# Performance work log

Hardware: AMD Instinct MI355X
Metric: run time of the kernel (lower is better)

The kernel has to match this reference:

```python
import jax, jax.numpy as jnp
import numpy as np

C_Z = 128
C_H = 128
N = 512
B = 1

def _layer_norm(x, g, b, eps=1e-5):
    mu = jnp.mean(x, axis=-1, keepdims=True)
    var = jnp.var(x, axis=-1, keepdims=True)
    return (x - mu) * jax.lax.rsqrt(var + eps) * g + b

def _linear(x, w, b):
    # torch Linear: y = x @ w.T + b, w: [out, in]
    return jnp.einsum('...i,oi->...o', x, w) + b

def setup_inputs() -> dict:
    key = jax.random.key(0)
    ks = jax.random.split(key, 8)
    s = 1.0 / np.sqrt(C_Z)
    return {
        'z': jax.random.normal(ks[0], (B, N, N, C_Z), jnp.float32),
        'mask': jnp.ones((B, N, N), jnp.float32),
        'ln_in_g': jnp.ones((C_Z,), jnp.float32),
        'ln_in_b': jnp.zeros((C_Z,), jnp.float32),
        'w_ag': jax.random.normal(ks[1], (C_H, C_Z), jnp.float32) * s,
        'b_ag': jnp.ones((C_H,), jnp.float32),
        'w_ap': jax.random.normal(ks[2], (C_H, C_Z), jnp.float32) * s,
        'b_ap': jnp.zeros((C_H,), jnp.float32),
        'w_bg': jax.random.normal(ks[3], (C_H, C_Z), jnp.float32) * s,
        'b_bg': jnp.ones((C_H,), jnp.float32),
        'w_bp': jax.random.normal(ks[4], (C_H, C_Z), jnp.float32) * s,
        'b_bp': jnp.zeros((C_H,), jnp.float32),
        'w_g': jax.random.normal(ks[5], (C_Z, C_Z), jnp.float32) * s,
        'b_g': jnp.zeros((C_Z,), jnp.float32),
        'w_z': jax.random.normal(ks[6], (C_Z, C_H), jnp.float32) * s,
        'b_z': jnp.zeros((C_Z,), jnp.float32),
        'ln_out_g': jnp.ones((C_H,), jnp.float32),
        'ln_out_b': jnp.zeros((C_H,), jnp.float32),
    }

def reference(z, mask, ln_in_g, ln_in_b, w_ag, b_ag, w_ap, b_ap,
              w_bg, b_bg, w_bp, b_bp, w_g, b_g, w_z, b_z,
              ln_out_g, ln_out_b):
    m = mask[..., None]                       # [B,N,N,1]
    zn = _layer_norm(z, ln_in_g, ln_in_b)     # [B,N,N,Cz]
    a = m * jax.nn.sigmoid(_linear(zn, w_ag, b_ag)) * _linear(zn, w_ap, b_ap)
    b = m * jax.nn.sigmoid(_linear(zn, w_bg, b_bg)) * _linear(zn, w_bp, b_bp)
    # outgoing: x[b,i,j,c] = sum_k a[b,i,k,c] * b[b,j,k,c]
    x = jnp.einsum('bikc,bjkc->bijc', a, b)
    x = _layer_norm(x, ln_out_g, ln_out_b)
    x = _linear(x, w_z, b_z)
    g = jax.nn.sigmoid(_linear(zn, w_g, b_g))
    return x * g
```

## Files before the change

kernel.cpp:

```cpp
#include <hip/hip_runtime.h>

#define NN 512
#define CCH 128
#define MM (NN*NN)

using f32x4  = __attribute__((ext_vector_type(4))) float;
using f32x2  = __attribute__((ext_vector_type(2))) float;
using f16x8  = __attribute__((ext_vector_type(8))) _Float16;
using u16x4  = __attribute__((ext_vector_type(4))) unsigned short;
using u32x2  = __attribute__((ext_vector_type(2))) unsigned int;
using u32x4  = __attribute__((ext_vector_type(4))) unsigned int;
typedef unsigned short u16;

__device__ __forceinline__ u16 f2h(float f) {
    return __builtin_bit_cast(u16, (_Float16)f);
}
__device__ __forceinline__ float h2f(u16 h) {
    return (float)__builtin_bit_cast(_Float16, h);
}
__device__ __forceinline__ unsigned pack2(float lo, float hi) {
    return (unsigned)f2h(lo) | ((unsigned)f2h(hi) << 16);
}
__device__ __forceinline__ float fsig_mul(float x, float y) {
    float e = __builtin_amdgcn_exp2f(x * -1.44269504f);
    return y * __builtin_amdgcn_rcpf(1.0f + e);
}
__device__ __forceinline__ float fsig(float x) {
    float e = __builtin_amdgcn_exp2f(x * -1.44269504f);
    return __builtin_amdgcn_rcpf(1.0f + e);
}

__device__ __forceinline__ void gl_lds16(const void* g, void* l) {
    __builtin_amdgcn_global_load_lds(
        (const __attribute__((address_space(1))) void*)g,
        (__attribute__((address_space(3))) void*)l, 16, 0, 0);
}

__global__ __launch_bounds__(256) void k_prep(
    const float* __restrict__ w0, const float* __restrict__ w1,
    const float* __restrict__ w2, const float* __restrict__ w3,
    const float* __restrict__ w4, const float* __restrict__ w5,
    const float* __restrict__ b0, const float* __restrict__ b1,
    const float* __restrict__ b2, const float* __restrict__ b3,
    const float* __restrict__ b4, const float* __restrict__ b5,
    const float* __restrict__ gin, const float* __restrict__ bin,
    const float* __restrict__ gout, const float* __restrict__ bout,
    u16* __restrict__ wbf, float* __restrict__ bias2) {
    int mat = blockIdx.x;
    const float* W = mat==0?w0:mat==1?w1:mat==2?w2:mat==3?w3:mat==4?w4:w5;
    const float* B = mat==0?b0:mat==1?b1:mat==2?b2:mat==3?b3:mat==4?b4:b5;
    const float* G = (mat==5)? gout : gin;
    const float* Bt= (mat==5)? bout : bin;
    __shared__ float gs[CCH], bs[CCH];
    int tid = threadIdx.x;
    if (tid < CCH) { gs[tid] = G[tid]; bs[tid] = Bt[tid]; }
    __syncthreads();
    int o = tid >> 1, c0 = (tid & 1) * 64;
    const float* src = W + o * CCH + c0;
    char* dstrow = (char*)(wbf + mat * 16384) + o * 256;
    int key = o & 7;
    float dot = 0.f;
    #pragma unroll
    for (int q = 0; q < 16; ++q) {
        f32x4 v = *(const f32x4*)(src + q * 4);
        int c = c0 + q * 4;
        dot += bs[c]*v.x + bs[c+1]*v.y + bs[c+2]*v.z + bs[c+3]*v.w;
        u16x4 p;
        p.x = f2h(v.x * gs[c]);     p.y = f2h(v.y * gs[c+1]);
        p.z = f2h(v.z * gs[c+2]);   p.w = f2h(v.w * gs[c+3]);
        int chunk = (c0 >> 3) + (q >> 1);
        *(u16x4*)(dstrow + (((chunk ^ key)) << 4) + ((q & 1) << 3)) = p;
    }
    dot += __shfl_xor(dot, 1);
    if ((tid & 1) == 0) bias2[mat * CCH + o] = B[o] + dot;
}

__global__ __launch_bounds__(512, 4) void k_fused(
    const float* __restrict__ z, const float* __restrict__ mask,
    const u16* __restrict__ wbf, const float* __restrict__ bias2,
    u16* __restrict__ aT, u16* __restrict__ bT, u16* gateB) {
    __shared__ __align__(16) u16 wls[32768];
    int tid = threadIdx.x, w = tid >> 6, lane = tid & 63;
    int r = lane & 15, kq = lane >> 4;
    long m0 = (long)blockIdx.x * 128;

    {
        const char* Wg = (const char*)wbf;
        #pragma unroll
        for (int it = 0; it < 8; ++it)
            gl_lds16(Wg + (long)it * 8192 + tid * 16, (char*)wls + it * 8192 + w * 1024);
    }

    long mrow = m0 + w * 16 + r;
    f16x8 av[4];
    {
        const float* zr = z + mrow * CCH;
        f32x4 zv[4][2];
        float s = 0.f, s2 = 0.f;
        #pragma unroll
        for (int kb = 0; kb < 4; ++kb) {
            zv[kb][0] = *(const f32x4*)(zr + kb * 32 + kq * 8);
            zv[kb][1] = *(const f32x4*)(zr + kb * 32 + kq * 8 + 4);
            #pragma unroll
            for (int h = 0; h < 2; ++h) {
                f32x4 v = zv[kb][h];
                s += v.x + v.y + v.z + v.w;
                s2 = fmaf(v.x, v.x, fmaf(v.y, v.y, fmaf(v.z, v.z, fmaf(v.w, v.w, s2))));
            }
        }
        s  += __shfl_xor(s, 16);  s  += __shfl_xor(s, 32);
        s2 += __shfl_xor(s2, 16); s2 += __shfl_xor(s2, 32);
        float mu = s * (1.0f / CCH);
        float var = fmaxf(s2 * (1.0f / CCH) - mu * mu, 0.f);
        float rs = rsqrtf(var + 1e-5f);
        #pragma unroll
        for (int kb = 0; kb < 4; ++kb) {
            f32x4 a0 = zv[kb][0], a1 = zv[kb][1];
            u32x4 o;
            o[0] = pack2((a0.x - mu) * rs, (a0.y - mu) * rs);
            o[1] = pack2((a0.z - mu) * rs, (a0.w - mu) * rs);
            o[2] = pack2((a1.x - mu) * rs, (a1.y - mu) * rs);
            o[3] = pack2((a1.z - mu) * rs, (a1.w - mu) * rs);
            av[kb] = __builtin_bit_cast(f16x8, o);
        }
    }
    f32x4 mkv = *(const f32x4*)(mask + m0 + w * 16 + kq * 4);

    float b1v[4][2], b2v[4][2];
    #pragma unroll
    for (int nt = 0; nt < 8; ++nt) {
        b1v[nt >> 1][nt & 1] = bias2[0 * CCH + nt * 16 + r];
        b2v[nt >> 1][nt & 1] = bias2[1 * CCH + nt * 16 + r];
    }

    int i7 = (int)((blockIdx.x >> 2) & 7);
    int q = w * 2 + (kq >> 1);
    long boff = m0 * 2 + ((long)(q >> 3) << 7) + ((long)((q & 7) ^ i7) << 4)
              + ((kq & 1) << 3);

    __syncthreads();

    f32x4 acc1[8], acc2[8];
    #pragma unroll
    for (int nt = 0; nt < 8; ++nt) { acc1[nt] = {0,0,0,0}; acc2[nt] = {0,0,0,0}; }
    #pragma unroll
    for (int nt = 0; nt < 8; ++nt) {
        int ol = nt * 16 + r;
        int key = ol & 7;
        const char* row1 = (const char*)wls + ol * 256;
        const char* row2 = (const char*)wls + 32768 + ol * 256;
        #pragma unroll
        for (int kb = 0; kb < 4; ++kb) {
            int ph16 = ((kb * 4 + kq) ^ key) << 4;
            f16x8 b1 = *(const f16x8*)(row1 + ph16);
            f16x8 b2 = *(const f16x8*)(row2 + ph16);
            acc1[nt] = __builtin_amdgcn_mfma_f32_16x16x32_f16(av[kb], b1, acc1[nt], 0, 0, 0);
            acc2[nt] = __builtin_amdgcn_mfma_f32_16x16x32_f16(av[kb], b2, acc2[nt], 0, 0, 0);
        }
    }
    __syncthreads();

    {
        const char* Wg = (const char*)wbf + 65536;
        #pragma unroll
        for (int it = 0; it < 8; ++it)
            gl_lds16(Wg + (long)it * 8192 + tid * 16, (char*)wls + it * 8192 + w * 1024);
    }

    #pragma unroll
    for (int nt = 0; nt < 8; ++nt) {
        int cc = nt * 16 + r;
        float bb1 = b1v[nt >> 1][nt & 1], bb2 = b2v[nt >> 1][nt & 1];
        float v0 = fsig_mul(acc1[nt][0] + bb1, mkv[0] * (acc2[nt][0] + bb2));
        float v1 = fsig_mul(acc1[nt][1] + bb1, mkv[1] * (acc2[nt][1] + bb2));
        float v2 = fsig_mul(acc1[nt][2] + bb1, mkv[2] * (acc2[nt][2] + bb2));
        float v3 = fsig_mul(acc1[nt][3] + bb1, mkv[3] * (acc2[nt][3] + bb2));
        u32x2 pv; pv.x = pack2(v0, v1); pv.y = pack2(v2, v3);
        *(u32x2*)((char*)aT + ((long)cc << 19) + boff) = pv;
    }
    #pragma unroll
    for (int nt = 0; nt < 8; ++nt) {
        b1v[nt >> 1][nt & 1] = bias2[2 * CCH + nt * 16 + r];
        b2v[nt >> 1][nt & 1] = bias2[3 * CCH + nt * 16 + r];
    }
    __syncthreads();

    #pragma unroll
    for (int nt = 0; nt < 8; ++nt) { acc1[nt] = {0,0,0,0}; acc2[nt] = {0,0,0,0}; }
    #pragma unroll
    for (int nt = 0; nt < 8; ++nt) {
        int ol = nt * 16 + r;
        int key = ol & 7;
        const char* row1 = (const char*)wls + ol * 256;
        const char* row2 = (const char*)wls + 32768 + ol * 256;
        #pragma unroll
        for (int kb = 0; kb < 4; ++kb) {
            int ph16 = ((kb * 4 + kq) ^ key) << 4;
            f16x8 b1 = *(const f16x8*)(row1 + ph16);
            f16x8 b2 = *(const f16x8*)(row2 + ph16);
            acc1[nt] = __builtin_amdgcn_mfma_f32_16x16x32_f16(av[kb], b1, acc1[nt], 0, 0, 0);
            acc2[nt] = __builtin_amdgcn_mfma_f32_16x16x32_f16(av[kb], b2, acc2[nt], 0, 0, 0);
        }
    }
    __syncthreads();

    {
        const char* Wg = (const char*)wbf + 131072;
        #pragma unroll
        for (int it = 0; it < 4; ++it)
            gl_lds16(Wg + (long)it * 8192 + tid * 16, (char*)wls + it * 8192 + w * 1024);
    }

    #pragma unroll
    for (int nt = 0; nt < 8; ++nt) {
        int cc = nt * 16 + r;
        float bb1 = b1v[nt >> 1][nt & 1], bb2 = b2v[nt >> 1][nt & 1];
        float v0 = fsig_mul(acc1[nt][0] + bb1, mkv[0] * (acc2[nt][0] + bb2));
        float v1 = fsig_mul(acc1[nt][1] + bb1, mkv[1] * (acc2[nt][1] + bb2));
        float v2 = fsig_mul(acc1[nt][2] + bb1, mkv[2] * (acc2[nt][2] + bb2));
        float v3 = fsig_mul(acc1[nt][3] + bb1, mkv[3] * (acc2[nt][3] + bb2));
        u32x2 pv; pv.x = pack2(v0, v1); pv.y = pack2(v2, v3);
        *(u32x2*)((char*)bT + ((long)cc << 19) + boff) = pv;
    }
    f32x4 bg[8];
    #pragma unroll
    for (int nt = 0; nt < 8; ++nt)
        bg[nt] = *(const f32x4*)(bias2 + 4 * CCH + nt * 16 + kq * 4);
    __syncthreads();

    {
        f32x4 acc[8];
        #pragma unroll
        for (int nt = 0; nt < 8; ++nt) acc[nt] = {0,0,0,0};
        #pragma unroll
        for (int nt = 0; nt < 8; ++nt) {
            int ol = nt * 16 + r;
            int key = ol & 7;
            const char* row1 = (const char*)wls + ol * 256;
            #pragma unroll
            for (int kb = 0; kb < 4; ++kb) {
                f16x8 b1 = *(const f16x8*)(row1 + (((kb * 4 + kq) ^ key) << 4));
                acc[nt] = __builtin_amdgcn_mfma_f32_16x16x32_f16(b1, av[kb], acc[nt], 0, 0, 0);
            }
        }
        #pragma unroll
        for (int nt = 0; nt < 8; ++nt) {
            int c0 = nt * 16 + kq * 4;
            u32x2 pv;
            pv.x = pack2(fsig(acc[nt][0] + bg[nt][0]), fsig(acc[nt][1] + bg[nt][1]));
            pv.y = pack2(fsig(acc[nt][2] + bg[nt][2]), fsig(acc[nt][3] + bg[nt][3]));
            *(u32x2*)(gateB + mrow * 256 + c0) = pv;
        }
    }
}

__global__ __launch_bounds__(256, 4) void k_tri(const u16* __restrict__ aT,
                                                const u16* __restrict__ bT,
                                                u16* __restrict__ xT) {
    __shared__ __align__(16) char shm[34816];
    u16* At = (u16*)shm;
    u16* Bt = (u16*)(shm + 16384);
    int tid = threadIdx.x;
    int w = tid >> 6, lane = tid & 63;
    int r = lane & 15, kq = lane >> 4;

    int L = blockIdx.x;
    int xcd = L & 7, idx = L >> 3;
    int c    = xcd + 8 * (idx >> 4);
    int tile = idx & 15;
    int ti = tile >> 2, tj = tile & 3;

    const char* abase = (const char*)(aT + (long)c * MM) + (long)(ti * 128) * 1024;
    const char* bbase = (const char*)(bT + (long)c * MM) + (long)(tj * 128) * 1024;
    int wm = w >> 1, wn = w & 1;

    f32x4 acc[4][4];
    #pragma unroll
    for (int a = 0; a < 4; ++a)
        #pragma unroll
        for (int bq = 0; bq < 4; ++bq) acc[a][bq] = {0.f,0.f,0.f,0.f};

    for (int ks = 0; ks < 8; ++ks) {
        const char* asrc = abase + ks * 128;
        const char* bsrc = bbase + ks * 128;
        #pragma unroll
        for (int it = 0; it < 4; ++it) {
            int u = it * 256 + tid;
            long goff = (long)(u >> 3) * 1024 + (u & 7) * 16;
            gl_lds16(asrc + goff, (char*)At + it * 4096 + w * 1024);
            gl_lds16(bsrc + goff, (char*)Bt + it * 4096 + w * 1024);
        }
        __syncthreads();

        #pragma unroll
        for (int kh = 0; kh < 2; ++kh) {
            f16x8 af[4];
            #pragma unroll
            for (int mt = 0; mt < 4; ++mt) {
                int rowa = wm * 64 + mt * 16 + r;
                af[mt] = *(const f16x8*)((const char*)At + rowa * 128 +
                                         (((kh * 4 + kq) ^ (r & 7)) << 4));
            }
            #pragma unroll
            for (int nt = 0; nt < 4; ++nt) {
                int rowb = wn * 64 + nt * 16 + r;
                f16x8 bf = *(const f16x8*)((const char*)Bt + rowb * 128 +
                                           (((kh * 4 + kq) ^ (r & 7)) << 4));
                #pragma unroll
                for (int mt = 0; mt < 4; ++mt)
                    acc[mt][nt] = __builtin_amdgcn_mfma_f32_16x16x32_f16(bf, af[mt], acc[mt][nt], 0, 0, 0);
            }
        }
        __syncthreads();
    }

    char* tb = shm;
    #pragma unroll
    for (int mt = 0; mt < 4; ++mt) {
        int il = wm * 64 + mt * 16 + r;
        #pragma unroll
        for (int nt = 0; nt < 4; ++nt) {
            int jl = wn * 64 + nt * 16 + kq * 4;
            u32x2 pv;
            pv.x = pack2(acc[mt][nt][0], acc[mt][nt][1]);
            pv.y = pack2(acc[mt][nt][2], acc[mt][nt][3]);
            *(u32x2*)(tb + il * 272 + jl * 2) = pv;
        }
    }
    __syncthreads();
    u16* xrow = xT + (long)c * MM + (long)(ti * 128) * NN + tj * 128;
    int joff = tid & 15;
    #pragma unroll
    for (int rd = 0; rd < 8; ++rd) {
        int il = rd * 16 + (tid >> 4);
        u32x4 vv = *(const u32x4*)(tb + il * 272 + joff * 16);
        *(u32x4*)(xrow + (long)il * NN + joff * 8) = vv;
    }
}

__global__ __launch_bounds__(256, 4) void k_out(const u16* __restrict__ xT,
                                                const u16* __restrict__ wbf,
                                                const float* __restrict__ bias2,
                                                const u16* gateB,
                                                float* __restrict__ outp) {
    __shared__ __align__(16) char shm[34816];
    u16* xl = (u16*)shm;
    int tid = threadIdx.x, w = tid >> 6, lane = tid & 63;
    int r = lane & 15, kq = lane >> 4;
    long m0 = (long)blockIdx.x * 64;

    {
        int cg = tid & 31, ms = tid >> 5;
        int c0 = cg * 4;
        const u16* base = xT + m0 + (long)ms * 8;
        u16x4 t;
        const u16* s0 = base + (long)(c0 + 0) * MM;
        const u16* s1 = base + (long)(c0 + 1) * MM;
        const u16* s2 = base + (long)(c0 + 2) * MM;
        const u16* s3 = base + (long)(c0 + 3) * MM;
        #pragma unroll
        for (int e = 0; e < 8; ++e) {
            int m = ms * 8 + e;
            t.x = s0[e]; t.y = s1[e]; t.z = s2[e]; t.w = s3[e];
            *(u16x4*)((char*)xl + m * 256 + ((c0 * 2) ^ ((m & 15) << 4))) = t;
        }
    }
    __syncthreads();

    int mlr = w * 16 + r;
    int swm = (mlr & 15) << 4;
    u32x4 avu[4];
    float s = 0.f, s2 = 0.f;
    #pragma unroll
    for (int kb = 0; kb < 4; ++kb) {
        avu[kb] = *(const u32x4*)((const char*)xl + mlr * 256 + ((kb * 64 + kq * 16) ^ swm));
        #pragma unroll
        for (int p = 0; p < 4; ++p) {
            unsigned u = avu[kb][p];
            float flo = h2f((u16)(u & 0xFFFFu));
            float fhi = h2f((u16)(u >> 16));
            s += flo + fhi;
            s2 = fmaf(flo, flo, s2);
            s2 = fmaf(fhi, fhi, s2);
        }
    }
    s  += __shfl_xor(s, 16);  s  += __shfl_xor(s, 32);
    s2 += __shfl_xor(s2, 16); s2 += __shfl_xor(s2, 32);
    float mu = s * (1.0f / CCH);
    float var = fmaxf(s2 * (1.0f / CCH) - mu * mu, 0.f);
    float rs = rsqrtf(var + 1e-5f);
    float nmu = -mu * rs;
    f16x8 av[4];
    #pragma unroll
    for (int kb = 0; kb < 4; ++kb) {
        u32x4 o;
        #pragma unroll
        for (int p = 0; p < 4; ++p) {
            unsigned u = avu[kb][p];
            float flo = h2f((u16)(u & 0xFFFFu));
            float fhi = h2f((u16)(u >> 16));
            o[p] = pack2(fmaf(flo, rs, nmu), fmaf(fhi, rs, nmu));
        }
        av[kb] = __builtin_bit_cast(f16x8, o);
    }

    long m = m0 + w * 16 + r;
    u16x4 gvu[8];
    f32x4 bb[8];
    #pragma unroll
    for (int nt = 0; nt < 8; ++nt) {
        gvu[nt] = *(const u16x4*)(gateB + m * 256 + nt * 16 + kq * 4);
        bb[nt]  = *(const f32x4*)(bias2 + 5 * CCH + nt * 16 + kq * 4);
    }

    const char* Wz = (const char*)(wbf + 5 * 16384);
    f32x4 acc[8];
    #pragma unroll
    for (int nt = 0; nt < 8; ++nt) acc[nt] = {0,0,0,0};
    #pragma unroll
    for (int nt = 0; nt < 8; ++nt) {
        int ol = nt * 16 + r;
        int key = ol & 7;
        const char* row = Wz + ol * 256;
        #pragma unroll
        for (int kb = 0; kb < 4; ++kb) {
            f16x8 bw = *(const f16x8*)(row + (((kb * 4 + kq) ^ key) << 4));
            acc[nt] = __builtin_amdgcn_mfma_f32_16x16x32_f16(bw, av[kb], acc[nt], 0, 0, 0);
        }
    }

    __syncthreads();

    {
        char* tile = shm;
        int ml = w * 16 + r;
        #pragma unroll
        for (int nt = 0; nt < 8; ++nt) {
            int c0 = nt * 16 + kq * 4;
            f32x4 o;
            #pragma unroll
            for (int j = 0; j < 4; ++j)
                o[j] = (acc[nt][j] + bb[nt][j]) * h2f(gvu[nt][j]);
            *(f32x4*)(tile + ml * 528 + c0 * 4) = o;
        }
    }
    __syncthreads();

    {
        const char* tile = shm;
        int part = tid & 31;
        #pragma unroll
        for (int rd = 0; rd < 8; ++rd) {
            int ml = rd * 8 + (tid >> 5);
            f32x4 v = *(const f32x4*)(tile + ml * 528 + part * 16);
            *(f32x4*)(outp + (m0 + ml) * CCH + part * 4) = v;
        }
    }
}

extern "C" void kernel_launch(void* const* d_in, const int* in_sizes, int n_in,
                              void* d_out, int out_size, void* d_ws, size_t ws_size,
                              hipStream_t stream) {
    const float* z       = (const float*)d_in[0];
    const float* mask    = (const float*)d_in[1];
    const float* ln_in_g = (const float*)d_in[2];
    const float* ln_in_b = (const float*)d_in[3];
    const float* w_ag    = (const float*)d_in[4];
    const float* b_ag    = (const float*)d_in[5];
    const float* w_ap    = (const float*)d_in[6];
    const float* b_ap    = (const float*)d_in[7];
    const float* w_bg    = (const float*)d_in[8];
    const float* b_bg    = (const float*)d_in[9];
    const float* w_bp    = (const float*)d_in[10];
    const float* b_bp    = (const float*)d_in[11];
    const float* w_g     = (const float*)d_in[12];
    const float* b_g     = (const float*)d_in[13];
    const float* w_z     = (const float*)d_in[14];
    const float* b_z     = (const float*)d_in[15];
    const float* ln_o_g  = (const float*)d_in[16];
    const float* ln_o_b  = (const float*)d_in[17];
    float* out = (float*)d_out;
    u16* gateB = (u16*)d_out;

    char* ws = (char*)d_ws;
    const size_t SL = (size_t)MM * CCH * 2;
    u16* xT   = (u16*)ws;
    u16* aT   = (u16*)(ws + SL);
    u16* bT   = (u16*)(ws + 2 * SL);
    u16* wbf  = (u16*)(ws + 3 * SL);
    float* b2 = (float*)(ws + 3 * SL + 6 * 16384 * 2);

    k_prep<<<6, 256, 0, stream>>>(w_ag, w_ap, w_bg, w_bp, w_g, w_z,
                                  b_ag, b_ap, b_bg, b_bp, b_g, b_z,
                                  ln_in_g, ln_in_b, ln_o_g, ln_o_b, wbf, b2);
    k_fused<<<MM / 128, 512, 0, stream>>>(z, mask, wbf, b2, aT, bT, gateB);
    k_tri<<<2048, 256, 0, stream>>>(aT, bT, xT);
    k_out<<<MM / 64, 256, 0, stream>>>(xT, wbf, b2, gateB, out);
}
```

Before: 287.9 us.

## Enlarge triangle-multiply tile to 128x256 with 512 threads and direct stores

```diff
diff --git a/kernel.cpp b/kernel.cpp
--- a/kernel.cpp
+++ b/kernel.cpp
@@ -254,25 +254,24 @@
     }
 }
 
-__global__ __launch_bounds__(256, 4) void k_tri(const u16* __restrict__ aT,
+__global__ __launch_bounds__(512, 4) void k_tri(const u16* __restrict__ aT,
                                                 const u16* __restrict__ bT,
                                                 u16* __restrict__ xT) {
-    __shared__ __align__(16) char shm[34816];
-    u16* At = (u16*)shm;
-    u16* Bt = (u16*)(shm + 16384);
+    __shared__ __align__(16) u16 At[128 * 64];
+    __shared__ __align__(16) u16 Bt[256 * 64];
     int tid = threadIdx.x;
     int w = tid >> 6, lane = tid & 63;
     int r = lane & 15, kq = lane >> 4;
 
     int L = blockIdx.x;
     int xcd = L & 7, idx = L >> 3;
-    int c    = xcd + 8 * (idx >> 4);
-    int tile = idx & 15;
-    int ti = tile >> 2, tj = tile & 3;
+    int c    = xcd + 8 * (idx >> 3);
+    int tile = idx & 7;
+    int ti = tile >> 1, tj = tile & 1;
 
     const char* abase = (const char*)(aT + (long)c * MM) + (long)(ti * 128) * 1024;
-    const char* bbase = (const char*)(bT + (long)c * MM) + (long)(tj * 128) * 1024;
-    int wm = w >> 1, wn = w & 1;
+    const char* bbase = (const char*)(bT + (long)c * MM) + (long)(tj * 256) * 1024;
+    int wi = w >> 2, wj = w & 3;
 
     f32x4 acc[4][4];
     #pragma unroll
@@ -284,11 +283,16 @@
         const char* asrc = abase + ks * 128;
         const char* bsrc = bbase + ks * 128;
         #pragma unroll
+        for (int it = 0; it < 2; ++it) {
+            int u = it * 512 + tid;
+            long goff = (long)(u >> 3) * 1024 + (u & 7) * 16;
+            gl_lds16(asrc + goff, (char*)At + it * 8192 + w * 1024);
+        }
+        #pragma unroll
         for (int it = 0; it < 4; ++it) {
-            int u = it * 256 + tid;
+            int u = it * 512 + tid;
             long goff = (long)(u >> 3) * 1024 + (u & 7) * 16;
-            gl_lds16(asrc + goff, (char*)At + it * 4096 + w * 1024);
-            gl_lds16(bsrc + goff, (char*)Bt + it * 4096 + w * 1024);
+            gl_lds16(bsrc + goff, (char*)Bt + it * 8192 + w * 1024);
         }
         __syncthreads();
 
@@ -297,13 +301,13 @@
             f16x8 af[4];
             #pragma unroll
             for (int mt = 0; mt < 4; ++mt) {
-                int rowa = wm * 64 + mt * 16 + r;
+                int rowa = wi * 64 + mt * 16 + r;
                 af[mt] = *(const f16x8*)((const char*)At + rowa * 128 +
                                          (((kh * 4 + kq) ^ (r & 7)) << 4));
             }
             #pragma unroll
             for (int nt = 0; nt < 4; ++nt) {
-                int rowb = wn * 64 + nt * 16 + r;
+                int rowb = wj * 64 + nt * 16 + r;
                 f16x8 bf = *(const f16x8*)((const char*)Bt + rowb * 128 +
                                            (((kh * 4 + kq) ^ (r & 7)) << 4));
                 #pragma unroll
@@ -314,27 +318,20 @@
         __syncthreads();
     }
 
-    char* tb = shm;
+    u16* xbase = xT + (long)c * MM;
+    int gi0 = ti * 128 + wi * 64;
+    int gj0 = tj * 256 + wj * 64;
     #pragma unroll
     for (int mt = 0; mt < 4; ++mt) {
-        int il = wm * 64 + mt * 16 + r;
+        long row = gi0 + mt * 16 + r;
         #pragma unroll
         for (int nt = 0; nt < 4; ++nt) {
-            int jl = wn * 64 + nt * 16 + kq * 4;
+            int col = gj0 + nt * 16 + kq * 4;
             u32x2 pv;
             pv.x = pack2(acc[mt][nt][0], acc[mt][nt][1]);
             pv.y = pack2(acc[mt][nt][2], acc[mt][nt][3]);
-            *(u32x2*)(tb + il * 272 + jl * 2) = pv;
-        }
-    }
-    __syncthreads();
-    u16* xrow = xT + (long)c * MM + (long)(ti * 128) * NN + tj * 128;
-    int joff = tid & 15;
-    #pragma unroll
-    for (int rd = 0; rd < 8; ++rd) {
-        int il = rd * 16 + (tid >> 4);
-        u32x4 vv = *(const u32x4*)(tb + il * 272 + joff * 16);
-        *(u32x4*)(xrow + (long)il * NN + joff * 8) = vv;
+            *(u32x2*)(xbase + row * NN + col) = pv;
+        }
     }
 }
 
@@ -494,6 +491,6 @@
                                   b_ag, b_ap, b_bg, b_bp, b_g, b_z,
                                   ln_in_g, ln_in_b, ln_o_g, ln_o_b, wbf, b2);
     k_fused<<<MM / 128, 512, 0, stream>>>(z, mask, wbf, b2, aT, bT, gateB);
-    k_tri<<<2048, 256, 0, stream>>>(aT, bT, xT);
+    k_tri<<<1024, 512, 0, stream>>>(aT, bT, xT);
     k_out<<<MM / 64, 256, 0, stream>>>(xT, wbf, b2, gateB, out);
 }
```

Result: slower. 295.1 us (+2.5%).
